# Performance work log

Hardware: AMD Instinct MI355X
Metric: run time of the kernel (lower is better)

The kernel has to match this reference:

```python
import jax, jax.numpy as jnp
import numpy as np

D_MODEL = 1024
NUM_HEADS = 16
HEAD_DIM = D_MODEL // NUM_HEADS
MAX_SEQ_LEN = 2048
THETA = 10000.0
BATCH = 2
SEQ = 2048


def _rope_tables():
    inv_freq = 1.0 / (THETA ** (jnp.arange(0, HEAD_DIM, 2, dtype=jnp.float32) / HEAD_DIM))
    pos = jnp.arange(MAX_SEQ_LEN, dtype=jnp.float32)
    freqs = pos[:, None] * inv_freq[None, :]  # [max_seq, head_dim/2]
    return jnp.sin(freqs), jnp.cos(freqs)


def _apply_rope(x, sin, cos):
    # x: [b, h, s, d]; sin/cos: [s, d/2] -> broadcast over b, h
    sin = sin[None, None, :, :]
    cos = cos[None, None, :, :]
    x_even = x[..., 0::2]
    x_odd = x[..., 1::2]
    out_even = x_even * cos - x_odd * sin
    out_odd = x_even * sin + x_odd * cos
    # interleave back: stack on new last axis then flatten
    out = jnp.stack((out_even, out_odd), axis=-1)
    return out.reshape(x.shape)


def setup_inputs() -> dict:
    key = jax.random.key(0)
    ks = jax.random.split(key, 5)
    std = (2.0 / (D_MODEL + D_MODEL)) ** 0.5
    return {
        "x": jax.random.normal(ks[0], (BATCH, SEQ, D_MODEL), dtype=jnp.float32),
        "Wq": jax.random.normal(ks[1], (D_MODEL, D_MODEL), dtype=jnp.float32) * std,
        "Wk": jax.random.normal(ks[2], (D_MODEL, D_MODEL), dtype=jnp.float32) * std,
        "Wv": jax.random.normal(ks[3], (D_MODEL, D_MODEL), dtype=jnp.float32) * std,
        "Wo": jax.random.normal(ks[4], (D_MODEL, D_MODEL), dtype=jnp.float32) * std,
    }


def reference(x, Wq, Wk, Wv, Wo):
    b, s, _ = x.shape
    # projections: weight stored [out, in] as in the torch Linear
    Q = jnp.einsum('bsd,od->bso', x, Wq)
    K = jnp.einsum('bsd,od->bso', x, Wk)
    V = jnp.einsum('bsd,od->bso', x, Wv)
    # split heads -> [b, h, s, hd]
    def split(t):
        return t.reshape(b, s, NUM_HEADS, HEAD_DIM).transpose(0, 2, 1, 3)
    Q, K, V = split(Q), split(K), split(V)
    sin, cos = _rope_tables()
    sin, cos = sin[:s], cos[:s]
    Q = _apply_rope(Q, sin, cos)
    K = _apply_rope(K, sin, cos)
    scale = 1.0 / jnp.sqrt(jnp.float32(HEAD_DIM))
    scores = jnp.einsum('bhqd,bhkd->bhqk', Q, K)
    causal = jnp.tril(jnp.ones((s, s), dtype=bool))[None, None]
    scores = jnp.where(causal, scores, -jnp.inf) * scale  # -inf * scale stays -inf
    attn = jax.nn.softmax(scores, axis=-1)
    out = jnp.einsum('bhqk,bhkd->bhqd', attn, V)
    out = out.transpose(0, 2, 1, 3).reshape(b, s, D_MODEL)
    return jnp.einsum('bsd,od->bso', out, Wo)
```

## Files before the change

### kernel.cpp

```cpp
#include <hip/hip_runtime.h>
#include <math.h>

#define NHEADS 16
#define HD 64
#define SEQ 2048
#define BATCH 2
#define DM 1024
#define MTOT (BATCH*SEQ)
#define LDP 72

typedef __bf16 bf16x8 __attribute__((ext_vector_type(8)));
typedef __bf16 bf16x4 __attribute__((ext_vector_type(4)));
typedef float  f32x4  __attribute__((ext_vector_type(4)));

#define LOG2E 1.4426950408889634f

#define GLD16(gp, lp) __builtin_amdgcn_global_load_lds( \
    (const __attribute__((address_space(1))) void*)(gp), \
    (__attribute__((address_space(3))) void*)(lp), 16, 0, 0)

__global__ __launch_bounds__(256)
void cast_all(const float* __restrict__ x, const float* __restrict__ Wq,
              const float* __restrict__ Wk, const float* __restrict__ Wv,
              const float* __restrict__ Wo,
              __bf16* __restrict__ xb, __bf16* __restrict__ Wqkvb,
              __bf16* __restrict__ Wob)
{
    const size_t NX = (size_t)MTOT * DM;
    const size_t NW = (size_t)DM * DM;
    const size_t i = ((size_t)blockIdx.x * 256 + threadIdx.x) * 8;
    const float* src; __bf16* dst; size_t off;
    if (i < NX)               { src = x;  dst = xb;           off = i; }
    else if (i < NX + NW)     { src = Wq; dst = Wqkvb;        off = i - NX; }
    else if (i < NX + 2*NW)   { src = Wk; dst = Wqkvb + NW;   off = i - NX - NW; }
    else if (i < NX + 3*NW)   { src = Wv; dst = Wqkvb + 2*NW; off = i - NX - 2*NW; }
    else                      { src = Wo; dst = Wob;          off = i - NX - 3*NW; }
    const float4 f0 = *(const float4*)&src[off];
    const float4 f1 = *(const float4*)&src[off + 4];
    bf16x8 o;
    o[0] = (__bf16)f0.x; o[1] = (__bf16)f0.y; o[2] = (__bf16)f0.z; o[3] = (__bf16)f0.w;
    o[4] = (__bf16)f1.x; o[5] = (__bf16)f1.y; o[6] = (__bf16)f1.z; o[7] = (__bf16)f1.w;
    *(bf16x8*)&dst[off] = o;
}

template<int BM, int BN, int MODE>
__global__ __launch_bounds__(256, 4)
void gemm_mfma(const __bf16* __restrict__ A, const __bf16* __restrict__ W,
               float* __restrict__ Cf,
               __bf16* __restrict__ Qb, __bf16* __restrict__ Kb,
               __bf16* __restrict__ Vtb)
{
    constexpr int IT = BM / 32;
    constexpr int JT = BN / 32;
    __shared__ __bf16 As[BM * 64];
    __shared__ __bf16 Bs[BN * 64];

    const int tid  = threadIdx.x;
    const int lane = tid & 63;
    const int wave = tid >> 6;
    const int ll   = lane & 15;
    const int quad = lane >> 4;
    const int wm   = (wave & 1) * (BM / 2);
    const int wn   = (wave >> 1) * (BN / 2);
    const int bm   = blockIdx.x * BM;
    const int bn   = blockIdx.y * BN;

    const __bf16* Ab = A + (size_t)bm * DM;
    const __bf16* Wb = W + (size_t)bn * DM;

    f32x4 acc[IT][JT];
#pragma unroll
    for (int i = 0; i < IT; i++)
#pragma unroll
        for (int j = 0; j < JT; j++) acc[i][j] = (f32x4){0.f, 0.f, 0.f, 0.f};

    for (int k0 = 0; k0 < DM; k0 += 64) {
#pragma unroll
        for (int j = 0; j < BM / 32; j++) {
            const int t = tid + 256 * j;
            const int r = t >> 3, g = t & 7;
            GLD16(Ab + (size_t)r * DM + k0 + ((g ^ (r & 7)) * 8), &As[t * 8]);
        }
#pragma unroll
        for (int j = 0; j < BN / 32; j++) {
            const int t = tid + 256 * j;
            const int r = t >> 3, g = t & 7;
            GLD16(Wb + (size_t)r * DM + k0 + ((g ^ (r & 7)) * 8), &Bs[t * 8]);
        }
        __syncthreads();

#pragma unroll
        for (int kh = 0; kh < 2; kh++) {
            bf16x8 af[IT], bfr[JT];
#pragma unroll
            for (int i = 0; i < IT; i++) {
                const int r = wm + i*16 + ll;
                const int g = kh*4 + quad;
                af[i] = *(const bf16x8*)&As[(r*8 + (g ^ (r & 7))) * 8];
            }
#pragma unroll
            for (int j = 0; j < JT; j++) {
                const int r = wn + j*16 + ll;
                const int g = kh*4 + quad;
                bfr[j] = *(const bf16x8*)&Bs[(r*8 + (g ^ (r & 7))) * 8];
            }
#pragma unroll
            for (int i = 0; i < IT; i++)
#pragma unroll
                for (int j = 0; j < JT; j++)
                    acc[i][j] = __builtin_amdgcn_mfma_f32_16x16x32_bf16(
                        af[i], bfr[j], acc[i][j], 0, 0, 0);
        }
        __syncthreads();
    }

    if (MODE == 1) {
#pragma unroll
        for (int i = 0; i < IT; i++) {
#pragma unroll
            for (int j = 0; j < JT; j++) {
                const int gc = bn + wn + j*16 + ll;
#pragma unroll
                for (int r = 0; r < 4; r++) {
                    const int gr = bm + wm + i*16 + quad*4 + r;
                    Cf[(size_t)gr * DM + gc] = acc[i][j][r];
                }
            }
        }
    } else {
        const int which = bn >> 10;
        const int nb = bn & 1023;
#pragma unroll
        for (int i = 0; i < IT; i++) {
            const int m0 = bm + wm + i*16 + quad*4;
            const int b  = m0 >> 11;
            const int s0 = m0 & (SEQ - 1);
#pragma unroll
            for (int j = 0; j < JT; j++) {
                const int n_g = nb + wn + j*16 + ll;
                const int h = n_g >> 6, d = n_g & (HD - 1);
                if (which == 2) {
                    bf16x4 pk;
#pragma unroll
                    for (int r = 0; r < 4; r++) pk[r] = (__bf16)acc[i][j][r];
                    *(bf16x4*)&Vtb[((size_t)((b*NHEADS + h)*HD + d)) * SEQ + s0] = pk;
                } else {
                    __bf16* P = (which == 0) ? Qb : Kb;
                    const float sc = (which == 0) ? 0.125f * LOG2E : 1.0f;
                    const float inv =
                        exp2f(-(float)(d & ~1) * (13.287712379549449f / 64.0f));
                    const bool odd = (d & 1);
#pragma unroll
                    for (int r = 0; r < 4; r++) {
                        const float own = acc[i][j][r];
                        const float oth = __shfl_xor(own, 1);
                        float sn, cs;
                        __sincosf((float)(s0 + r) * inv, &sn, &cs);
                        const float xe = odd ? oth : own;
                        const float xo = odd ? own : oth;
                        const float o = odd ? (xe * sn + xo * cs)
                                            : (xe * cs - xo * sn);
                        P[((size_t)(b*NHEADS + h) * SEQ + s0 + r) * HD + d] =
                            (__bf16)(o * sc);
                    }
                }
            }
        }
    }
}

__global__ __launch_bounds__(256, 2)
void attn_mfma(const __bf16* __restrict__ Qb, const __bf16* __restrict__ Kb,
               const __bf16* __restrict__ Vtb, __bf16* __restrict__ AOb)
{
    __shared__ __align__(16) __bf16 pt[4][16][LDP];
    __shared__ float comb[4][64][66];
    __shared__ float lbuf[4][64];

    const int tid  = threadIdx.x;
    const int wave = tid >> 6;
    const int lane = tid & 63;
    const int m    = lane & 15;
    const int quad = lane >> 4;
    const int bh   = blockIdx.x;
    const int b    = bh >> 4, h = bh & 15;

    const __bf16* Qp = Qb + (size_t)bh * SEQ * HD;
    const __bf16* Kp = Kb + (size_t)bh * SEQ * HD;
    const __bf16* Vp = Vtb + (size_t)bh * HD * SEQ;

    bf16x8 ones;
#pragma unroll
    for (int j = 0; j < 8; j++) ones[j] = (__bf16)1.0f;

#pragma unroll 1
    for (int pass = 0; pass < 2; pass++) {
        const int qb = pass ? (SEQ/64 - 1) - (int)blockIdx.y : (int)blockIdx.y;
        const int q0 = qb * 64;

        bf16x8 qf[4][2];
#pragma unroll
        for (int i = 0; i < 4; i++) {
            const __bf16* qp = Qp + (size_t)(q0 + i*16 + m) * HD + quad*8;
            qf[i][0] = *(const bf16x8*)qp;
            qf[i][1] = *(const bf16x8*)(qp + 32);
        }

        f32x4 acc[4][4];
        f32x4 l_acc[4];
#pragma unroll
        for (int i = 0; i < 4; i++) {
            l_acc[i] = (f32x4){0.f, 0.f, 0.f, 0.f};
#pragma unroll
            for (int nt = 0; nt < 4; nt++) acc[i][nt] = (f32x4){0.f, 0.f, 0.f, 0.f};
        }

        for (int t = wave; t <= qb; t += 4) {
            const int k0 = t * 64;
            const bool diag = (t == qb);

            bf16x8 kf[4][2], vf[4][2];
#pragma unroll
            for (int tk = 0; tk < 4; tk++) {
                const __bf16* kp = Kp + (size_t)(k0 + tk*16 + m) * HD + quad*8;
                kf[tk][0] = *(const bf16x8*)kp;
                kf[tk][1] = *(const bf16x8*)(kp + 32);
                const __bf16* vp = Vp + (size_t)(tk*16 + m) * SEQ + k0 + quad*8;
                vf[tk][0] = *(const bf16x8*)vp;
                vf[tk][1] = *(const bf16x8*)(vp + 32);
            }

#pragma unroll
            for (int i = 0; i < 4; i++) {
                f32x4 s[4];
#pragma unroll
                for (int tk = 0; tk < 4; tk++) {
                    s[tk] = (f32x4){0.f, 0.f, 0.f, 0.f};
                    s[tk] = __builtin_amdgcn_mfma_f32_16x16x32_bf16(
                        qf[i][0], kf[tk][0], s[tk], 0, 0, 0);
                    s[tk] = __builtin_amdgcn_mfma_f32_16x16x32_bf16(
                        qf[i][1], kf[tk][1], s[tk], 0, 0, 0);
                }
#pragma unroll
                for (int tk = 0; tk < 4; tk++) {
#pragma unroll
                    for (int r = 0; r < 4; r++) {
                        float sv = s[tk][r];
                        if (diag)
                            sv = (16*tk + m <= 16*i + quad*4 + r) ? sv : -INFINITY;
                        const float p = __builtin_amdgcn_exp2f(sv);
                        pt[wave][quad*4 + r][16*tk + m] = (__bf16)p;
                    }
                }
                const bf16x8 af0 = *(const bf16x8*)&pt[wave][m][quad*8];
                const bf16x8 af1 = *(const bf16x8*)&pt[wave][m][32 + quad*8];
                l_acc[i] = __builtin_amdgcn_mfma_f32_16x16x32_bf16(
                    af0, ones, l_acc[i], 0, 0, 0);
                l_acc[i] = __builtin_amdgcn_mfma_f32_16x16x32_bf16(
                    af1, ones, l_acc[i], 0, 0, 0);
#pragma unroll
                for (int nt = 0; nt < 4; nt++) {
                    acc[i][nt] = __builtin_amdgcn_mfma_f32_16x16x32_bf16(
                        af0, vf[nt][0], acc[i][nt], 0, 0, 0);
                    acc[i][nt] = __builtin_amdgcn_mfma_f32_16x16x32_bf16(
                        af1, vf[nt][1], acc[i][nt], 0, 0, 0);
                }
            }
        }

        __syncthreads();
#pragma unroll
        for (int i = 0; i < 4; i++) {
#pragma unroll
            for (int nt = 0; nt < 4; nt++)
#pragma unroll
                for (int r = 0; r < 4; r++)
                    comb[wave][i*16 + quad*4 + r][nt*16 + m] = acc[i][nt][r];
            if (m == 0)
#pragma unroll
                for (int r = 0; r < 4; r++)
                    lbuf[wave][i*16 + quad*4 + r] = l_acc[i][r];
        }
        __syncthreads();

        {
            const int row = tid >> 2;
            const int cg  = (tid & 3) * 16;
            const float l = lbuf[0][row] + lbuf[1][row] + lbuf[2][row] + lbuf[3][row];
            const float rl = 1.0f / l;
            __bf16* op = AOb + (size_t)(b * SEQ + q0 + row) * DM + h * HD + cg;
#pragma unroll
            for (int c = 0; c < 16; c++) {
                const float o = comb[0][row][cg + c] + comb[1][row][cg + c]
                              + comb[2][row][cg + c] + comb[3][row][cg + c];
                op[c] = (__bf16)(o * rl);
            }
        }
        __syncthreads();
    }
}

extern "C" void kernel_launch(void* const* d_in, const int* in_sizes, int n_in,
                              void* d_out, int out_size, void* d_ws, size_t ws_size,
                              hipStream_t stream) {
    const float* x  = (const float*)d_in[0];
    const float* Wq = (const float*)d_in[1];
    const float* Wk = (const float*)d_in[2];
    const float* Wv = (const float*)d_in[3];
    const float* Wo = (const float*)d_in[4];
    float* out = (float*)d_out;

    char* ws = (char*)d_ws;
    __bf16* xb    = (__bf16*)ws;
    __bf16* Wqkvb = (__bf16*)(ws + ((size_t)8  << 20));
    __bf16* Wob   = (__bf16*)(ws + ((size_t)14 << 20));
    __bf16* Qb    = (__bf16*)(ws + ((size_t)16 << 20));
    __bf16* Kb    = (__bf16*)(ws + ((size_t)24 << 20));
    __bf16* Vtb   = (__bf16*)(ws + ((size_t)32 << 20));
    __bf16* AOb   = (__bf16*)(ws + ((size_t)40 << 20));

    cast_all<<<4096, 256, 0, stream>>>(x, Wq, Wk, Wv, Wo, xb, Wqkvb, Wob);

    gemm_mfma<64,128,0><<<dim3(MTOT/64, 3072/128), 256, 0, stream>>>(
        xb, Wqkvb, nullptr, Qb, Kb, Vtb);

    attn_mfma<<<dim3(BATCH*NHEADS, SEQ/128), 256, 0, stream>>>(Qb, Kb, Vtb, AOb);

    gemm_mfma<64,64,1><<<dim3(MTOT/64, DM/64), 256, 0, stream>>>(
        AOb, Wob, out, nullptr, nullptr, nullptr);
}
```

Baseline: 174.0 us.

## Split attention passes into separate blocks and shrink LDS for higher occupancy

The two causal-balanced query-block passes per workgroup become two separate workgroups via a z grid dimension. The cross-wave combine buffer shrinks from a full 64x66 tile to a 64x17 slice reused over four column chunks, and launch bounds rise to 4 blocks per CU. The aim is more resident waves and more parallel blocks to hide latency, at the cost of extra barriers in the epilogue, possible register pressure from the tighter bound, and less load balance per block since each now handles one query block.

Measured after the change: 305.0 us. 75.3% more time.

```diff
diff --git a/kernel.cpp b/kernel.cpp
--- a/kernel.cpp
+++ b/kernel.cpp
@@ -169,12 +169,12 @@
     }
 }
 
-__global__ __launch_bounds__(256, 2)
+__global__ __launch_bounds__(256, 4)
 void attn_mfma(const __bf16* __restrict__ Qb, const __bf16* __restrict__ Kb,
                const __bf16* __restrict__ Vtb, __bf16* __restrict__ AOb)
 {
     __shared__ __align__(16) __bf16 pt[4][16][LDP];
-    __shared__ float comb[4][64][66];
+    __shared__ float comb[4][64][17];
     __shared__ float lbuf[4][64];
 
     const int tid  = threadIdx.x;
@@ -184,6 +184,8 @@
     const int quad = lane >> 4;
     const int bh   = blockIdx.x;
     const int b    = bh >> 4, h = bh & 15;
+    const int qb   = blockIdx.z ? (SEQ/64 - 1) - (int)blockIdx.y : (int)blockIdx.y;
+    const int q0   = qb * 64;
 
     const __bf16* Qp = Qb + (size_t)bh * SEQ * HD;
     const __bf16* Kp = Kb + (size_t)bh * SEQ * HD;
@@ -193,110 +195,109 @@
 #pragma unroll
     for (int j = 0; j < 8; j++) ones[j] = (__bf16)1.0f;
 
-#pragma unroll 1
-    for (int pass = 0; pass < 2; pass++) {
-        const int qb = pass ? (SEQ/64 - 1) - (int)blockIdx.y : (int)blockIdx.y;
-        const int q0 = qb * 64;
-
-        bf16x8 qf[4][2];
+    bf16x8 qf[4][2];
+#pragma unroll
+    for (int i = 0; i < 4; i++) {
+        const __bf16* qp = Qp + (size_t)(q0 + i*16 + m) * HD + quad*8;
+        qf[i][0] = *(const bf16x8*)qp;
+        qf[i][1] = *(const bf16x8*)(qp + 32);
+    }
+
+    f32x4 acc[4][4];
+    f32x4 l_acc[4];
+#pragma unroll
+    for (int i = 0; i < 4; i++) {
+        l_acc[i] = (f32x4){0.f, 0.f, 0.f, 0.f};
+#pragma unroll
+        for (int nt = 0; nt < 4; nt++) acc[i][nt] = (f32x4){0.f, 0.f, 0.f, 0.f};
+    }
+
+    for (int t = wave; t <= qb; t += 4) {
+        const int k0 = t * 64;
+        const bool diag = (t == qb);
+
+        bf16x8 kf[4][2], vf[4][2];
+#pragma unroll
+        for (int tk = 0; tk < 4; tk++) {
+            const __bf16* kp = Kp + (size_t)(k0 + tk*16 + m) * HD + quad*8;
+            kf[tk][0] = *(const bf16x8*)kp;
+            kf[tk][1] = *(const bf16x8*)(kp + 32);
+            const __bf16* vp = Vp + (size_t)(tk*16 + m) * SEQ + k0 + quad*8;
+            vf[tk][0] = *(const bf16x8*)vp;
+            vf[tk][1] = *(const bf16x8*)(vp + 32);
+        }
+
 #pragma unroll
         for (int i = 0; i < 4; i++) {
-            const __bf16* qp = Qp + (size_t)(q0 + i*16 + m) * HD + quad*8;
-            qf[i][0] = *(const bf16x8*)qp;
-            qf[i][1] = *(const bf16x8*)(qp + 32);
-        }
-
-        f32x4 acc[4][4];
-        f32x4 l_acc[4];
-#pragma unroll
-        for (int i = 0; i < 4; i++) {
-            l_acc[i] = (f32x4){0.f, 0.f, 0.f, 0.f};
-#pragma unroll
-            for (int nt = 0; nt < 4; nt++) acc[i][nt] = (f32x4){0.f, 0.f, 0.f, 0.f};
-        }
-
-        for (int t = wave; t <= qb; t += 4) {
-            const int k0 = t * 64;
-            const bool diag = (t == qb);
-
-            bf16x8 kf[4][2], vf[4][2];
+            f32x4 s[4];
 #pragma unroll
             for (int tk = 0; tk < 4; tk++) {
-                const __bf16* kp = Kp + (size_t)(k0 + tk*16 + m) * HD + quad*8;
-                kf[tk][0] = *(const bf16x8*)kp;
-                kf[tk][1] = *(const bf16x8*)(kp + 32);
-                const __bf16* vp = Vp + (size_t)(tk*16 + m) * SEQ + k0 + quad*8;
-                vf[tk][0] = *(const bf16x8*)vp;
-                vf[tk][1] = *(const bf16x8*)(vp + 32);
-            }
-
-#pragma unroll
-            for (int i = 0; i < 4; i++) {
-                f32x4 s[4];
-#pragma unroll
-                for (int tk = 0; tk < 4; tk++) {
-                    s[tk] = (f32x4){0.f, 0.f, 0.f, 0.f};
-                    s[tk] = __builtin_amdgcn_mfma_f32_16x16x32_bf16(
-                        qf[i][0], kf[tk][0], s[tk], 0, 0, 0);
-                    s[tk] = __builtin_amdgcn_mfma_f32_16x16x32_bf16(
-                        qf[i][1], kf[tk][1], s[tk], 0, 0, 0);
+                s[tk] = (f32x4){0.f, 0.f, 0.f, 0.f};
+                s[tk] = __builtin_amdgcn_mfma_f32_16x16x32_bf16(
+                    qf[i][0], kf[tk][0], s[tk], 0, 0, 0);
+                s[tk] = __builtin_amdgcn_mfma_f32_16x16x32_bf16(
+                    qf[i][1], kf[tk][1], s[tk], 0, 0, 0);
+            }
+#pragma unroll
+            for (int tk = 0; tk < 4; tk++) {
+#pragma unroll
+                for (int r = 0; r < 4; r++) {
+                    float sv = s[tk][r];
+                    if (diag)
+                        sv = (16*tk + m <= 16*i + quad*4 + r) ? sv : -INFINITY;
+                    const float p = __builtin_amdgcn_exp2f(sv);
+                    pt[wave][quad*4 + r][16*tk + m] = (__bf16)p;
                 }
-#pragma unroll
-                for (int tk = 0; tk < 4; tk++) {
-#pragma unroll
-                    for (int r = 0; r < 4; r++) {
-                        float sv = s[tk][r];
-                        if (diag)
-                            sv = (16*tk + m <= 16*i + quad*4 + r) ? sv : -INFINITY;
-                        const float p = __builtin_amdgcn_exp2f(sv);
-                        pt[wave][quad*4 + r][16*tk + m] = (__bf16)p;
-                    }
-                }
-                const bf16x8 af0 = *(const bf16x8*)&pt[wave][m][quad*8];
-                const bf16x8 af1 = *(const bf16x8*)&pt[wave][m][32 + quad*8];
-                l_acc[i] = __builtin_amdgcn_mfma_f32_16x16x32_bf16(
-                    af0, ones, l_acc[i], 0, 0, 0);
-                l_acc[i] = __builtin_amdgcn_mfma_f32_16x16x32_bf16(
-                    af1, ones, l_acc[i], 0, 0, 0);
-#pragma unroll
-                for (int nt = 0; nt < 4; nt++) {
-                    acc[i][nt] = __builtin_amdgcn_mfma_f32_16x16x32_bf16(
-                        af0, vf[nt][0], acc[i][nt], 0, 0, 0);
-                    acc[i][nt] = __builtin_amdgcn_mfma_f32_16x16x32_bf16(
-                        af1, vf[nt][1], acc[i][nt], 0, 0, 0);
-                }
-            }
-        }
-
+            }
+            const bf16x8 af0 = *(const bf16x8*)&pt[wave][m][quad*8];
+            const bf16x8 af1 = *(const bf16x8*)&pt[wave][m][32 + quad*8];
+            l_acc[i] = __builtin_amdgcn_mfma_f32_16x16x32_bf16(
+                af0, ones, l_acc[i], 0, 0, 0);
+            l_acc[i] = __builtin_amdgcn_mfma_f32_16x16x32_bf16(
+                af1, ones, l_acc[i], 0, 0, 0);
+#pragma unroll
+            for (int nt = 0; nt < 4; nt++) {
+                acc[i][nt] = __builtin_amdgcn_mfma_f32_16x16x32_bf16(
+                    af0, vf[nt][0], acc[i][nt], 0, 0, 0);
+                acc[i][nt] = __builtin_amdgcn_mfma_f32_16x16x32_bf16(
+                    af1, vf[nt][1], acc[i][nt], 0, 0, 0);
+            }
+        }
+    }
+
+    if (m == 0) {
+#pragma unroll
+        for (int i = 0; i < 4; i++)
+#pragma unroll
+            for (int r = 0; r < 4; r++)
+                lbuf[wave][i*16 + quad*4 + r] = l_acc[i][r];
+    }
+    __syncthreads();
+
+    const int row = tid >> 2;
+    const int c0  = (tid & 3) * 4;
+    const float rl = 1.0f / (lbuf[0][row] + lbuf[1][row]
+                           + lbuf[2][row] + lbuf[3][row]);
+    __bf16* op = AOb + (size_t)(b * SEQ + q0 + row) * DM + h * HD;
+
+#pragma unroll
+    for (int nt = 0; nt < 4; nt++) {
+#pragma unroll
+        for (int i = 0; i < 4; i++)
+#pragma unroll
+            for (int r = 0; r < 4; r++)
+                comb[wave][i*16 + quad*4 + r][m] = acc[i][nt][r];
         __syncthreads();
-#pragma unroll
-        for (int i = 0; i < 4; i++) {
-#pragma unroll
-            for (int nt = 0; nt < 4; nt++)
-#pragma unroll
-                for (int r = 0; r < 4; r++)
-                    comb[wave][i*16 + quad*4 + r][nt*16 + m] = acc[i][nt][r];
-            if (m == 0)
-#pragma unroll
-                for (int r = 0; r < 4; r++)
-                    lbuf[wave][i*16 + quad*4 + r] = l_acc[i][r];
-        }
-        __syncthreads();
-
-        {
-            const int row = tid >> 2;
-            const int cg  = (tid & 3) * 16;
-            const float l = lbuf[0][row] + lbuf[1][row] + lbuf[2][row] + lbuf[3][row];
-            const float rl = 1.0f / l;
-            __bf16* op = AOb + (size_t)(b * SEQ + q0 + row) * DM + h * HD + cg;
-#pragma unroll
-            for (int c = 0; c < 16; c++) {
-                const float o = comb[0][row][cg + c] + comb[1][row][cg + c]
-                              + comb[2][row][cg + c] + comb[3][row][cg + c];
-                op[c] = (__bf16)(o * rl);
-            }
-        }
-        __syncthreads();
+        bf16x4 ov;
+#pragma unroll
+        for (int cc = 0; cc < 4; cc++) {
+            const int col = c0 + cc;
+            const float o = comb[0][row][col] + comb[1][row][col]
+                          + comb[2][row][col] + comb[3][row][col];
+            ov[cc] = (__bf16)(o * rl);
+        }
+        *(bf16x4*)&op[nt*16 + c0] = ov;
+        if (nt < 3) __syncthreads();
     }
 }
 
@@ -324,7 +325,8 @@
     gemm_mfma<64,128,0><<<dim3(MTOT/64, 3072/128), 256, 0, stream>>>(
         xb, Wqkvb, nullptr, Qb, Kb, Vtb);
 
-    attn_mfma<<<dim3(BATCH*NHEADS, SEQ/128), 256, 0, stream>>>(Qb, Kb, Vtb, AOb);
+    attn_mfma<<<dim3(BATCH*NHEADS, SEQ/128, 2), 256, 0, stream>>>(
+        Qb, Kb, Vtb, AOb);
 
     gemm_mfma<64,64,1><<<dim3(MTOT/64, DM/64), 256, 0, stream>>>(
         AOb, Wob, out, nullptr, nullptr, nullptr);
```
